# Kernel tuning notes

Measured on AMD Instinct MI355X. Metric: run time of the kernel, lower is better.

The kernel has to match this reference:

```python
import jax, jax.numpy as jnp
import numpy as np

B, T, D = 1, 4096, 768
H, HD = 12, 64  # num_heads, head_dim; H*HD == D


def setup_inputs() -> dict:
    key = jax.random.key(0)
    ks = jax.random.split(key, 12)
    s = 1.0 / np.sqrt(D)  # nn.Linear-style init scale
    inp = {
        "query": jax.random.normal(ks[0], (B, T, D), jnp.float32),
        "key": jax.random.normal(ks[1], (B, T, D), jnp.float32),
        "value": jax.random.normal(ks[2], (B, T, D), jnp.float32),
        # causal mask: True positions are masked (strict upper triangle)
        "mask": jnp.triu(jnp.ones((T, T), dtype=bool), k=1),
        "Wq_w": jax.random.normal(ks[3], (D, D), jnp.float32) * s,
        "Wq_b": jax.random.normal(ks[4], (D,), jnp.float32) * s,
        "Wk_w": jax.random.normal(ks[5], (D, D), jnp.float32) * s,
        "Wk_b": jax.random.normal(ks[6], (D,), jnp.float32) * s,
        "Wv_w": jax.random.normal(ks[7], (D, D), jnp.float32) * s,
        "Wv_b": jax.random.normal(ks[8], (D,), jnp.float32) * s,
        "W0_w": jax.random.normal(ks[9], (D, D), jnp.float32) * s,
        "W0_b": jax.random.normal(ks[10], (D,), jnp.float32) * s,
    }
    return inp


def _split_heads(x):
    # (B, T, D) -> (B, H, T, HD)
    b, t, _ = x.shape
    return x.reshape(b, t, H, HD).transpose(0, 2, 1, 3)


def reference(query, key, value, mask, Wq_w, Wq_b, Wk_w, Wk_b, Wv_w, Wv_b, W0_w, W0_b):
    # Q/K/V projections (torch Linear: x @ W.T + b)
    q = _split_heads(query @ Wq_w.T + Wq_b)
    k = _split_heads(key @ Wk_w.T + Wk_b)
    v = _split_heads(value @ Wv_w.T + Wv_b)

    scale = 1.0 / jnp.sqrt(jnp.asarray(HD, q.dtype))
    scores = jnp.einsum("bhqd,bhkd->bhqk", q, k) * scale  # (B,H,T,T)
    scores = jnp.where(mask, -jnp.inf, scores)
    weights = jax.nn.softmax(scores, axis=-1)  # (B,H,T,T)
    attn = jnp.einsum("bhqk,bhkd->bhqd", weights, v)  # (B,H,T,HD)

    # concat heads: (B,H,T,HD) -> (B,T,D), then output projection
    out = attn.transpose(0, 2, 1, 3).reshape(query.shape[0], -1, D)
    output = out @ W0_w.T + W0_b
    return output, weights
```

## Files before the change

kernel.cpp:

```cpp
#include <hip/hip_runtime.h>

#define TSEQ 4096
#define DM 768
#define NHEAD 12
#define HDIM 64
#define SC 0.1803368801111204f

using f32x4  = __attribute__((ext_vector_type(4))) float;
using bf16x8 = __attribute__((ext_vector_type(8))) short;
using bf16x4 = __attribute__((ext_vector_type(4))) short;

#define LGKM_BARRIER() asm volatile("s_waitcnt lgkmcnt(0)\n\ts_barrier" ::: "memory")

__device__ __forceinline__ short f2bf(float f) {
    union { float f; unsigned u; } x; x.f = f;
    unsigned r = x.u + 0x7FFFu + ((x.u >> 16) & 1u);
    return (short)(r >> 16);
}

__device__ __forceinline__ unsigned pk2(float lo, float hi) {
    unsigned d;
    asm("v_cvt_pk_bf16_f32 %0, %1, %2" : "=v"(d) : "v"(lo), "v"(hi));
    return d;
}

__device__ __forceinline__ bf16x8 pack8(f32x4 a, f32x4 b) {
    union { unsigned u[4]; bf16x8 v; } r;
    r.u[0] = pk2(a[0], a[1]); r.u[1] = pk2(a[2], a[3]);
    r.u[2] = pk2(b[0], b[1]); r.u[3] = pk2(b[2], b[3]);
    return r.v;
}

__device__ __forceinline__ f32x4 mfma16(bf16x8 a, bf16x8 b, f32x4 c) {
    return __builtin_amdgcn_mfma_f32_16x16x32_bf16(a, b, c, 0, 0, 0);
}

__global__ __launch_bounds__(512) void gemm_qkv(
    const float* __restrict__ q_in, const float* __restrict__ k_in,
    const float* __restrict__ v_in,
    const float* __restrict__ Wq_w, const float* __restrict__ Wq_b,
    const float* __restrict__ Wk_w, const float* __restrict__ Wk_b,
    const float* __restrict__ Wv_w, const float* __restrict__ Wv_b,
    short* __restrict__ Qb, short* __restrict__ Kb, short* __restrict__ Vt)
{
    constexpr int K = DM;
    __shared__ __align__(16) short As[64 * 72];
    __shared__ __align__(16) short Bs[256 * 72];

    const int D = blockIdx.x;
    const int o = (D & 7) * 72 + (D >> 3);
    const int bm = (o & 63) * 64;
    const int g  = o >> 6;
    const int bn = (g % 3) * 256;
    const int z  = g / 3;

    const float* A    = (z == 0) ? q_in : (z == 1) ? k_in : v_in;
    const float* W    = (z == 0) ? Wq_w : (z == 1) ? Wk_w : Wv_w;
    const float* bias = (z == 0) ? Wq_b : (z == 1) ? Wk_b : Wv_b;

    const int tid = threadIdx.x;
    const int wid = tid >> 6;
    const int lane = tid & 63;
    const int wm = wid >> 2, wn = wid & 3;
    const int l15 = lane & 15, lq = lane >> 4;

    f32x4 acc[2][4] = {};
    const int sr = tid >> 3;
    const int sc = (tid & 7) * 8;

    for (int k0 = 0; k0 < K; k0 += 64) {
        {
            const float* ga = A + (size_t)(bm + sr) * K + k0 + sc;
            *(bf16x8*)&As[sr * 72 + sc] =
                pack8(*(const f32x4*)ga, *(const f32x4*)(ga + 4));
        }
        #pragma unroll
        for (int it = 0; it < 4; ++it) {
            int r = sr + it * 64;
            const float* gb = W + (size_t)(bn + r) * K + k0 + sc;
            *(bf16x8*)&Bs[r * 72 + sc] =
                pack8(*(const f32x4*)gb, *(const f32x4*)(gb + 4));
        }
        LGKM_BARRIER();
        __builtin_amdgcn_s_setprio(1);
        #pragma unroll
        for (int ks = 0; ks < 2; ++ks) {
            bf16x8 af0 = *(bf16x8*)&As[(wm * 32 + l15) * 72 + ks * 32 + lq * 8];
            bf16x8 af1 = *(bf16x8*)&As[(wm * 32 + 16 + l15) * 72 + ks * 32 + lq * 8];
            #pragma unroll
            for (int n = 0; n < 4; ++n) {
                bf16x8 bfv = *(bf16x8*)&Bs[(wn * 64 + n * 16 + l15) * 72 + ks * 32 + lq * 8];
                acc[0][n] = mfma16(af0, bfv, acc[0][n]);
                acc[1][n] = mfma16(af1, bfv, acc[1][n]);
            }
        }
        __builtin_amdgcn_s_setprio(0);
        LGKM_BARRIER();
    }

    #pragma unroll
    for (int mf = 0; mf < 2; ++mf) {
        const int row0 = bm + wm * 32 + mf * 16 + lq * 4;
        #pragma unroll
        for (int n = 0; n < 4; ++n) {
            int col = bn + wn * 64 + n * 16 + l15;
            float b = bias[col];
            if (z == 2) {
                uint2 pv;
                pv.x = pk2(acc[mf][n][0] + b, acc[mf][n][1] + b);
                pv.y = pk2(acc[mf][n][2] + b, acc[mf][n][3] + b);
                *(uint2*)(Vt + (size_t)col * TSEQ + row0) = pv;
            } else {
                short* dst = (z == 0) ? Qb : Kb;
                #pragma unroll
                for (int r = 0; r < 4; ++r)
                    dst[(size_t)(row0 + r) * DM + col] = f2bf(acc[mf][n][r] + b);
            }
        }
    }
}

__global__ __launch_bounds__(512) void gemm_out(
    const float* __restrict__ A, const float* __restrict__ W,
    const float* __restrict__ bias, float* __restrict__ Cout)
{
    constexpr int K = DM;
    __shared__ __align__(16) short As[64 * 72];
    __shared__ __align__(16) short Bs[256 * 72];

    const int D = blockIdx.x;
    const int o = (D & 7) * 24 + (D >> 3);
    const int bm = (o & 63) * 64;
    const int bn = (o >> 6) * 256;

    const int tid = threadIdx.x;
    const int wid = tid >> 6;
    const int lane = tid & 63;
    const int wm = wid >> 2, wn = wid & 3;
    const int l15 = lane & 15, lq = lane >> 4;

    f32x4 acc[2][4] = {};
    const int sr = tid >> 3;
    const int sc = (tid & 7) * 8;

    for (int k0 = 0; k0 < K; k0 += 64) {
        {
            const float* ga = A + (size_t)(bm + sr) * K + k0 + sc;
            *(bf16x8*)&As[sr * 72 + sc] =
                pack8(*(const f32x4*)ga, *(const f32x4*)(ga + 4));
        }
        #pragma unroll
        for (int it = 0; it < 4; ++it) {
            int r = sr + it * 64;
            const float* gb = W + (size_t)(bn + r) * K + k0 + sc;
            *(bf16x8*)&Bs[r * 72 + sc] =
                pack8(*(const f32x4*)gb, *(const f32x4*)(gb + 4));
        }
        LGKM_BARRIER();
        __builtin_amdgcn_s_setprio(1);
        #pragma unroll
        for (int ks = 0; ks < 2; ++ks) {
            bf16x8 af0 = *(bf16x8*)&As[(wm * 32 + l15) * 72 + ks * 32 + lq * 8];
            bf16x8 af1 = *(bf16x8*)&As[(wm * 32 + 16 + l15) * 72 + ks * 32 + lq * 8];
            #pragma unroll
            for (int n = 0; n < 4; ++n) {
                bf16x8 bfv = *(bf16x8*)&Bs[(wn * 64 + n * 16 + l15) * 72 + ks * 32 + lq * 8];
                acc[0][n] = mfma16(af0, bfv, acc[0][n]);
                acc[1][n] = mfma16(af1, bfv, acc[1][n]);
            }
        }
        __builtin_amdgcn_s_setprio(0);
        LGKM_BARRIER();
    }

    #pragma unroll
    for (int mf = 0; mf < 2; ++mf) {
        const int row0 = bm + wm * 32 + mf * 16 + lq * 4;
        #pragma unroll
        for (int n = 0; n < 4; ++n) {
            int col = bn + wn * 64 + n * 16 + l15;
            float b = bias[col];
            #pragma unroll
            for (int r = 0; r < 4; ++r)
                Cout[(size_t)(row0 + r) * DM + col] = acc[mf][n][r] + b;
        }
    }
}

__global__ __launch_bounds__(256) void attn_fused(
    const short* __restrict__ Qb, const short* __restrict__ Kb,
    const short* __restrict__ Vt, float* __restrict__ Wout,
    float* __restrict__ AttnO)
{
    const int qt = 63 - blockIdx.x;
    const int h = blockIdx.y;
    const int q0 = qt * 64;
    const int tid = threadIdx.x, wid = tid >> 6, lane = tid & 63;
    const int l15 = lane & 15, lq = lane >> 4;

    __shared__ __align__(16) short lds[23040];

    const int nkt = qt + 1;

    {
        float* wbase = Wout + (size_t)h * TSEQ * TSEQ + (size_t)(q0 + wid * 16) * TSEQ;
        f32x4 z = {0.f, 0.f, 0.f, 0.f};
        for (int kt = nkt; kt < 64; ++kt) {
            #pragma unroll
            for (int i = 0; i < 4; ++i)
                __builtin_nontemporal_store(
                    z, (f32x4*)(wbase + (size_t)(lq + i * 4) * TSEQ + kt * 64 + l15 * 4));
        }
    }

    const short* qp = Qb + (size_t)(q0 + wid * 16 + l15) * DM + h * HDIM + lq * 8;
    bf16x8 qf0 = *(const bf16x8*)qp;
    bf16x8 qf1 = *(const bf16x8*)(qp + 32);

    const short* kbase = Kb + (size_t)h * HDIM;
    const short* vbase = Vt + (size_t)h * HDIM * TSEQ;
    const int myq = q0 + wid * 16 + l15;

    const int srow = tid >> 3;
    const int scol = (tid & 7) * 8;

    const int nch = (nkt + 1) >> 1;
    auto stageKbig = [&](int c, int b) {
        const int base_k = c * 128;
        const int iters = (nkt * 64 - base_k) >= 128 ? 4 : 2;
        short* dst = lds + b * (128 * 72);
        for (int it = 0; it < iters; ++it) {
            int r = srow + it * 32;
            *(bf16x8*)&dst[r * 72 + scol] =
                *(const bf16x8*)&kbase[(size_t)(base_k + r) * DM + scol];
        }
    };

    f32x4 lacc = {0.f, 0.f, 0.f, 0.f};
    stageKbig(0, 0);
    LGKM_BARRIER();
    for (int c = 0; c < nch; ++c) {
        const int b = c & 1;
        if (c + 1 < nch) stageKbig(c + 1, b ^ 1);
        const short* kb = lds + b * (128 * 72);
        #pragma unroll
        for (int t = 0; t < 2; ++t) {
            const int kt = c * 2 + t;
            if (kt >= nkt) break;
            f32x4 s[4] = {};
            __builtin_amdgcn_s_setprio(1);
            #pragma unroll
            for (int ks = 0; ks < 2; ++ks) {
                bf16x8 qf = ks ? qf1 : qf0;
                #pragma unroll
                for (int n = 0; n < 4; ++n) {
                    bf16x8 kf = *(const bf16x8*)
                        &kb[(t * 64 + n * 16 + l15) * 72 + ks * 32 + lq * 8];
                    s[n] = mfma16(kf, qf, s[n]);
                }
            }
            __builtin_amdgcn_s_setprio(0);
            if (kt == qt) {
                #pragma unroll
                for (int n = 0; n < 4; ++n) {
                    int kb0 = kt * 64 + n * 16 + lq * 4;
                    #pragma unroll
                    for (int r = 0; r < 4; ++r)
                        lacc[n] += (kb0 + r <= myq) ? exp2f(s[n][r] * SC) : 0.f;
                }
            } else {
                #pragma unroll
                for (int n = 0; n < 4; ++n)
                    #pragma unroll
                    for (int r = 0; r < 4; ++r)
                        lacc[n] += exp2f(s[n][r] * SC);
            }
        }
        LGKM_BARRIER();
    }
    float lsum = (lacc[0] + lacc[1]) + (lacc[2] + lacc[3]);
    lsum += __shfl_xor(lsum, 16);
    lsum += __shfl_xor(lsum, 32);
    const float nlog = -__log2f(lsum);

    short* Ks2 = lds;
    short* Vs2 = lds + 2 * 64 * 72;
    short* Psw = lds + 4 * 64 * 72 + wid * (16 * 72);

    bf16x8 krg0, krg1, vrg0, vrg1;
    auto loadKV = [&](int kt) {
        krg0 = *(const bf16x8*)&kbase[(size_t)(kt * 64 + srow) * DM + scol];
        krg1 = *(const bf16x8*)&kbase[(size_t)(kt * 64 + srow + 32) * DM + scol];
        vrg0 = *(const bf16x8*)&vbase[(size_t)srow * TSEQ + kt * 64 + scol];
        vrg1 = *(const bf16x8*)&vbase[(size_t)(srow + 32) * TSEQ + kt * 64 + scol];
    };
    auto writeKV = [&](int b) {
        short* kd = Ks2 + b * (64 * 72);
        short* vd = Vs2 + b * (64 * 72);
        *(bf16x8*)&kd[srow * 72 + scol] = krg0;
        *(bf16x8*)&kd[(srow + 32) * 72 + scol] = krg1;
        *(bf16x8*)&vd[srow * 72 + scol] = vrg0;
        *(bf16x8*)&vd[(srow + 32) * 72 + scol] = vrg1;
    };

    float* wq = Wout + (size_t)h * TSEQ * TSEQ + (size_t)myq * TSEQ;
    f32x4 o[4] = {};
    loadKV(0);
    writeKV(0);
    LGKM_BARRIER();
    for (int kt = 0; kt < nkt; ++kt) {
        const int b = kt & 1;
        const bool more = (kt + 1 < nkt);
        if (more) {
            loadKV(kt + 1);
            __builtin_amdgcn_sched_barrier(0);
        }
        f32x4 s[4] = {};
        __builtin_amdgcn_s_setprio(1);
        #pragma unroll
        for (int ks = 0; ks < 2; ++ks) {
            bf16x8 qf = ks ? qf1 : qf0;
            #pragma unroll
            for (int n = 0; n < 4; ++n) {
                bf16x8 kf = *(const bf16x8*)
                    &Ks2[b * (64 * 72) + (n * 16 + l15) * 72 + ks * 32 + lq * 8];
                s[n] = mfma16(kf, qf, s[n]);
            }
        }
        __builtin_amdgcn_s_setprio(0);
        const bool diag = (kt == qt);
        #pragma unroll
        for (int n = 0; n < 4; ++n) {
            const int kb0 = kt * 64 + n * 16 + lq * 4;
            f32x4 p;
            #pragma unroll
            for (int r = 0; r < 4; ++r) {
                float e = exp2f(fmaf(s[n][r], SC, nlog));
                p[r] = (diag && (kb0 + r > myq)) ? 0.f : e;
            }
            *(f32x4*)(wq + kb0) = p;
            uint2 pv;
            pv.x = pk2(p[0], p[1]);
            pv.y = pk2(p[2], p[3]);
            *(uint2*)&Psw[l15 * 72 + n * 16 + lq * 4] = pv;
        }
        __builtin_amdgcn_s_setprio(1);
        #pragma unroll
        for (int ks = 0; ks < 2; ++ks) {
            bf16x8 pf = *(bf16x8*)&Psw[l15 * 72 + ks * 32 + lq * 8];
            #pragma unroll
            for (int n = 0; n < 4; ++n) {
                bf16x8 vf = *(const bf16x8*)
                    &Vs2[b * (64 * 72) + (n * 16 + l15) * 72 + ks * 32 + lq * 8];
                o[n] = mfma16(pf, vf, o[n]);
            }
        }
        __builtin_amdgcn_s_setprio(0);
        if (more) {
            __builtin_amdgcn_sched_barrier(0);
            writeKV(b ^ 1);
        }
        LGKM_BARRIER();
    }

    #pragma unroll
    for (int n = 0; n < 4; ++n) {
        int col = h * HDIM + n * 16 + l15;
        #pragma unroll
        for (int r = 0; r < 4; ++r) {
            int row = q0 + wid * 16 + lq * 4 + r;
            AttnO[(size_t)row * DM + col] = o[n][r];
        }
    }
}

extern "C" void kernel_launch(void* const* d_in, const int* in_sizes, int n_in,
                              void* d_out, int out_size, void* d_ws, size_t ws_size,
                              hipStream_t stream)
{
    const float* q_in = (const float*)d_in[0];
    const float* k_in = (const float*)d_in[1];
    const float* v_in = (const float*)d_in[2];
    const float* Wq_w = (const float*)d_in[4];
    const float* Wq_b = (const float*)d_in[5];
    const float* Wk_w = (const float*)d_in[6];
    const float* Wk_b = (const float*)d_in[7];
    const float* Wv_w = (const float*)d_in[8];
    const float* Wv_b = (const float*)d_in[9];
    const float* W0_w = (const float*)d_in[10];
    const float* W0_b = (const float*)d_in[11];

    float* out  = (float*)d_out;
    float* wout = out + (size_t)TSEQ * DM;

    short* Qb = (short*)d_ws;
    short* Kb = Qb + (size_t)TSEQ * DM;
    short* Vt = Kb + (size_t)TSEQ * DM;
    float* AttnO = (float*)(Vt + (size_t)TSEQ * DM);

    gemm_qkv<<<576, 512, 0, stream>>>(
        q_in, k_in, v_in, Wq_w, Wq_b, Wk_w, Wk_b, Wv_w, Wv_b, Qb, Kb, Vt);
    attn_fused<<<dim3(64, NHEAD), 256, 0, stream>>>(Qb, Kb, Vt, wout, AttnO);
    gemm_out<<<192, 512, 0, stream>>>(AttnO, W0_w, W0_b, out);
}
```

Measured before the change: 319.1 us.

## Enlarge attention query tile to 128 rows with 8 waves sharing K/V staging

The fused attention kernel now processes 128 query rows per block with 512 threads (8 waves), halving the grid and sharing each staged K/V tile across twice as many waves. This cuts redundant global loads of K and V across blocks. Per-wave diagonal handling (ktd) lets the top four waves skip the final key tile and just write zeros to the weights. The trade-offs are fewer blocks for load balancing on the causal triangle, more LDS per block, and some idle waves at the diagonal.

```diff
diff --git a/kernel.cpp b/kernel.cpp
--- a/kernel.cpp
+++ b/kernel.cpp
@@ -187,20 +187,21 @@
     }
 }
 
-__global__ __launch_bounds__(256) void attn_fused(
+__global__ __launch_bounds__(512) void attn_fused(
     const short* __restrict__ Qb, const short* __restrict__ Kb,
     const short* __restrict__ Vt, float* __restrict__ Wout,
     float* __restrict__ AttnO)
 {
-    const int qt = 63 - blockIdx.x;
+    const int qt = 31 - blockIdx.x;
     const int h = blockIdx.y;
-    const int q0 = qt * 64;
+    const int q0 = qt * 128;
     const int tid = threadIdx.x, wid = tid >> 6, lane = tid & 63;
     const int l15 = lane & 15, lq = lane >> 4;
 
-    __shared__ __align__(16) short lds[23040];
-
-    const int nkt = qt + 1;
+    __shared__ __align__(16) short lds[27648];
+
+    const int nkt = 2 * qt + 2;
+    const int ktd = 2 * qt + (wid >> 2);
 
     {
         float* wbase = Wout + (size_t)h * TSEQ * TSEQ + (size_t)(q0 + wid * 16) * TSEQ;
@@ -221,18 +222,17 @@
     const short* vbase = Vt + (size_t)h * HDIM * TSEQ;
     const int myq = q0 + wid * 16 + l15;
 
-    const int srow = tid >> 3;
+    const int sr   = tid >> 3;
     const int scol = (tid & 7) * 8;
 
-    const int nch = (nkt + 1) >> 1;
+    const int nch = qt + 1;
     auto stageKbig = [&](int c, int b) {
-        const int base_k = c * 128;
-        const int iters = (nkt * 64 - base_k) >= 128 ? 4 : 2;
         short* dst = lds + b * (128 * 72);
-        for (int it = 0; it < iters; ++it) {
-            int r = srow + it * 32;
+        #pragma unroll
+        for (int it = 0; it < 2; ++it) {
+            int r = sr + it * 64;
             *(bf16x8*)&dst[r * 72 + scol] =
-                *(const bf16x8*)&kbase[(size_t)(base_k + r) * DM + scol];
+                *(const bf16x8*)&kbase[(size_t)(c * 128 + r) * DM + scol];
         }
     };
 
@@ -245,8 +245,8 @@
         const short* kb = lds + b * (128 * 72);
         #pragma unroll
         for (int t = 0; t < 2; ++t) {
-            const int kt = c * 2 + t;
-            if (kt >= nkt) break;
+            const int kt = 2 * c + t;
+            if (kt > ktd) break;
             f32x4 s[4] = {};
             __builtin_amdgcn_s_setprio(1);
             #pragma unroll
@@ -260,7 +260,7 @@
                 }
             }
             __builtin_amdgcn_s_setprio(0);
-            if (kt == qt) {
+            if (kt == ktd) {
                 #pragma unroll
                 for (int n = 0; n < 4; ++n) {
                     int kb0 = kt * 64 + n * 16 + lq * 4;
@@ -287,20 +287,14 @@
     short* Vs2 = lds + 2 * 64 * 72;
     short* Psw = lds + 4 * 64 * 72 + wid * (16 * 72);
 
-    bf16x8 krg0, krg1, vrg0, vrg1;
+    bf16x8 krg, vrg;
     auto loadKV = [&](int kt) {
-        krg0 = *(const bf16x8*)&kbase[(size_t)(kt * 64 + srow) * DM + scol];
-        krg1 = *(const bf16x8*)&kbase[(size_t)(kt * 64 + srow + 32) * DM + scol];
-        vrg0 = *(const bf16x8*)&vbase[(size_t)srow * TSEQ + kt * 64 + scol];
-        vrg1 = *(const bf16x8*)&vbase[(size_t)(srow + 32) * TSEQ + kt * 64 + scol];
+        krg = *(const bf16x8*)&kbase[(size_t)(kt * 64 + sr) * DM + scol];
+        vrg = *(const bf16x8*)&vbase[(size_t)sr * TSEQ + kt * 64 + scol];
     };
     auto writeKV = [&](int b) {
-        short* kd = Ks2 + b * (64 * 72);
-        short* vd = Vs2 + b * (64 * 72);
-        *(bf16x8*)&kd[srow * 72 + scol] = krg0;
-        *(bf16x8*)&kd[(srow + 32) * 72 + scol] = krg1;
-        *(bf16x8*)&vd[srow * 72 + scol] = vrg0;
-        *(bf16x8*)&vd[(srow + 32) * 72 + scol] = vrg1;
+        *(bf16x8*)&Ks2[b * (64 * 72) + sr * 72 + scol] = krg;
+        *(bf16x8*)&Vs2[b * (64 * 72) + sr * 72 + scol] = vrg;
     };
 
     float* wq = Wout + (size_t)h * TSEQ * TSEQ + (size_t)myq * TSEQ;
@@ -315,47 +309,53 @@
             loadKV(kt + 1);
             __builtin_amdgcn_sched_barrier(0);
         }
-        f32x4 s[4] = {};
-        __builtin_amdgcn_s_setprio(1);
-        #pragma unroll
-        for (int ks = 0; ks < 2; ++ks) {
-            bf16x8 qf = ks ? qf1 : qf0;
+        if (kt <= ktd) {
+            f32x4 s[4] = {};
+            __builtin_amdgcn_s_setprio(1);
+            #pragma unroll
+            for (int ks = 0; ks < 2; ++ks) {
+                bf16x8 qf = ks ? qf1 : qf0;
+                #pragma unroll
+                for (int n = 0; n < 4; ++n) {
+                    bf16x8 kf = *(const bf16x8*)
+                        &Ks2[b * (64 * 72) + (n * 16 + l15) * 72 + ks * 32 + lq * 8];
+                    s[n] = mfma16(kf, qf, s[n]);
+                }
+            }
+            __builtin_amdgcn_s_setprio(0);
             #pragma unroll
             for (int n = 0; n < 4; ++n) {
-                bf16x8 kf = *(const bf16x8*)
-                    &Ks2[b * (64 * 72) + (n * 16 + l15) * 72 + ks * 32 + lq * 8];
-                s[n] = mfma16(kf, qf, s[n]);
-            }
-        }
-        __builtin_amdgcn_s_setprio(0);
-        const bool diag = (kt == qt);
-        #pragma unroll
-        for (int n = 0; n < 4; ++n) {
-            const int kb0 = kt * 64 + n * 16 + lq * 4;
-            f32x4 p;
-            #pragma unroll
-            for (int r = 0; r < 4; ++r) {
-                float e = exp2f(fmaf(s[n][r], SC, nlog));
-                p[r] = (diag && (kb0 + r > myq)) ? 0.f : e;
-            }
-            *(f32x4*)(wq + kb0) = p;
-            uint2 pv;
-            pv.x = pk2(p[0], p[1]);
-            pv.y = pk2(p[2], p[3]);
-            *(uint2*)&Psw[l15 * 72 + n * 16 + lq * 4] = pv;
-        }
-        __builtin_amdgcn_s_setprio(1);
-        #pragma unroll
-        for (int ks = 0; ks < 2; ++ks) {
-            bf16x8 pf = *(bf16x8*)&Psw[l15 * 72 + ks * 32 + lq * 8];
-            #pragma unroll
-            for (int n = 0; n < 4; ++n) {
-                bf16x8 vf = *(const bf16x8*)
-                    &Vs2[b * (64 * 72) + (n * 16 + l15) * 72 + ks * 32 + lq * 8];
-                o[n] = mfma16(pf, vf, o[n]);
-            }
-        }
-        __builtin_amdgcn_s_setprio(0);
+                const int kb0 = kt * 64 + n * 16 + lq * 4;
+                f32x4 p;
+                #pragma unroll
+                for (int r = 0; r < 4; ++r) {
+                    float e = exp2f(fmaf(s[n][r], SC, nlog));
+                    p[r] = (kb0 + r > myq) ? 0.f : e;
+                }
+                *(f32x4*)(wq + kb0) = p;
+                uint2 pv;
+                pv.x = pk2(p[0], p[1]);
+                pv.y = pk2(p[2], p[3]);
+                *(uint2*)&Psw[l15 * 72 + n * 16 + lq * 4] = pv;
+            }
+            __builtin_amdgcn_s_setprio(1);
+            #pragma unroll
+            for (int ks = 0; ks < 2; ++ks) {
+                bf16x8 pf = *(bf16x8*)&Psw[l15 * 72 + ks * 32 + lq * 8];
+                #pragma unroll
+                for (int n = 0; n < 4; ++n) {
+                    bf16x8 vf = *(const bf16x8*)
+                        &Vs2[b * (64 * 72) + (n * 16 + l15) * 72 + ks * 32 + lq * 8];
+                    o[n] = mfma16(pf, vf, o[n]);
+                }
+            }
+            __builtin_amdgcn_s_setprio(0);
+        } else {
+            f32x4 z = {0.f, 0.f, 0.f, 0.f};
+            #pragma unroll
+            for (int n = 0; n < 4; ++n)
+                *(f32x4*)(wq + kt * 64 + n * 16 + lq * 4) = z;
+        }
         if (more) {
             __builtin_amdgcn_sched_barrier(0);
             writeKV(b ^ 1);
@@ -400,6 +400,6 @@
 
     gemm_qkv<<<576, 512, 0, stream>>>(
         q_in, k_in, v_in, Wq_w, Wq_b, Wk_w, Wk_b, Wv_w, Wv_b, Qb, Kb, Vt);
-    attn_fused<<<dim3(64, NHEAD), 256, 0, stream>>>(Qb, Kb, Vt, wout, AttnO);
+    attn_fused<<<dim3(32, NHEAD), 512, 0, stream>>>(Qb, Kb, Vt, wout, AttnO);
     gemm_out<<<192, 512, 0, stream>>>(AttnO, W0_w, W0_b, out);
 }
```

New measurement: 340.7 us. 6.8% more time.
